# Kernel tuning notes

Measured on AMD Instinct MI355X. Metric: run time of the kernel, lower is better.

Reference implementation:

```python
import jax, jax.numpy as jnp
import numpy as np

N = 4096; IN = 78; OUT = 11
HN = 256; HB = 128; HM = 64; HV = 256; HU = 128
NOTES_PER_BEAT = 8; BEATS_PER_MEASURE = 4
NB = N // NOTES_PER_BEAT; NM = NB // BEATS_PER_MEASURE
UIN = 2*HN + 2*HB + 2*HM + 2*HV + OUT + 2 + 1 + 2   # output-LSTM input = 1424
BT_IN = 2*HB + 1 + 1 + 2 + 3 + (OUT - 1)            # tempo-LSTM input = 273
QPM_PRIMO_IDX = 5; TEMPO_IDX = 28


def _u(key, shape, k):
    return jax.random.uniform(key, shape, minval=-k, maxval=k, dtype=jnp.float32)


def _lstm_p(key, din, h, bidir):
    k = 1.0 / np.sqrt(h); n = 2 if bidir else 1
    k1, k2, k3 = jax.random.split(key, 3)
    Wi = _u(k1, (n, 4*h, din), k); Wh = _u(k2, (n, 4*h, h), k); b = _u(k3, (n, 4*h), k)
    if not bidir:
        Wi, Wh, b = Wi[0], Wh[0], b[0]
    return Wi, Wh, b


def _lin_p(key, din, dout):
    k = 1.0 / np.sqrt(din)
    k1, k2 = jax.random.split(key)
    return _u(k1, (dout, din), k), _u(k2, (dout,), k)


def setup_inputs():
    ks = jax.random.split(jax.random.key(0), 20)
    inp = {}
    inp['x'] = jax.random.normal(ks[0], (1, N, IN), dtype=jnp.float32)
    inp['y'] = jax.random.normal(ks[1], (1, 1, OUT), dtype=jnp.float32)
    inp['beat_ids'] = (jnp.arange(N) // NOTES_PER_BEAT).astype(jnp.int32)
    inp['measure_ids'] = (jnp.arange(N) // (NOTES_PER_BEAT * BEATS_PER_MEASURE)).astype(jnp.int32)
    inp['note_Wi'], inp['note_Wh'], inp['note_b'] = _lstm_p(ks[2], IN, HN, True)
    inp['voice_Wi'], inp['voice_Wh'], inp['voice_b'] = _lstm_p(ks[3], IN, HV, True)
    inp['beat_Wi'], inp['beat_Wh'], inp['beat_b'] = _lstm_p(ks[4], 2*HN, HB, True)
    inp['meas_Wi'], inp['meas_Wh'], inp['meas_b'] = _lstm_p(ks[5], 2*HB, HM, True)
    inp['Wba'], inp['bba'] = _lin_p(ks[6], 2*HN, 2*HN)
    inp['Wma'], inp['bma'] = _lin_p(ks[7], 2*HB, 2*HB)
    inp['Wta'], inp['bta'] = _lin_p(ks[8], OUT-1, OUT-1)
    inp['out_Wi'], inp['out_Wh'], inp['out_b'] = _lstm_p(ks[9], UIN, HU, False)
    inp['Wfc'], inp['bfc'] = _lin_p(ks[10], HU + UIN, OUT-1)
    inp['bt_Wi'], inp['bt_Wh'], inp['bt_b'] = _lstm_p(ks[11], BT_IN, HB, False)
    inp['Wt1'], inp['bt1'] = _lin_p(ks[12], HB, HB)
    inp['Wt2'], inp['bt2'] = _lin_p(ks[13], HB, 1)
    return inp


def _cell(h, c, xt, Wi, Wh, b):
    g = Wi @ xt + Wh @ h + b
    i, f, gg, o = jnp.split(g, 4)
    c2 = jax.nn.sigmoid(f) * c + jax.nn.sigmoid(i) * jnp.tanh(gg)
    return jax.nn.sigmoid(o) * jnp.tanh(c2), c2


def _lstm(xs, Wi, Wh, b, reverse=False):
    H = Wh.shape[-1]
    def step(carry, xt):
        h, c = _cell(carry[0], carry[1], xt, Wi, Wh, b)
        return (h, c), h
    init = (jnp.zeros(H, xs.dtype), jnp.zeros(H, xs.dtype))
    _, hs = jax.lax.scan(step, init, xs, reverse=reverse)
    return hs


def _bilstm(xs, Wi, Wh, b):
    return jnp.concatenate([_lstm(xs, Wi[0], Wh[0], b[0]),
                            _lstm(xs, Wi[1], Wh[1], b[1], reverse=True)], axis=-1)


def _seg_attn(h, seg, nseg, W, b):
    # sum_with_attention: softmax over group members, per feature dim (torch softmax dim=0)
    logits = h @ W.T + b
    m = jax.ops.segment_max(logits, seg, num_segments=nseg)
    e = jnp.exp(logits - m[seg])
    s = jax.ops.segment_sum(e, seg, num_segments=nseg)
    return jax.ops.segment_sum(h * (e / s[seg]), seg, num_segments=nseg)


def _forward(x, y, beat_ids, measure_ids, note_Wi, note_Wh, note_b, voice_Wi, voice_Wh, voice_b,
             beat_Wi, beat_Wh, beat_b, meas_Wi, meas_Wh, meas_b, Wba, bba, Wma, bma, Wta, bta,
             out_Wi, out_Wh, out_b, Wfc, bfc, bt_Wi, bt_Wh, bt_b, Wt1, bt1, Wt2, bt2):
    xs = x[0]                                   # [N, IN]
    note_h = _bilstm(xs, note_Wi, note_Wh, note_b)          # [N, 2*HN]
    voice_h = _bilstm(xs, voice_Wi, voice_Wh, voice_b)      # single voice -> whole seq
    beat_nodes = _seg_attn(note_h, beat_ids, NB, Wba, bba)  # [NB, 2*HN]
    beat_h = _bilstm(beat_nodes, beat_Wi, beat_Wh, beat_b)  # [NB, 2*HB]
    meas_of_beat = jax.ops.segment_min(measure_ids, beat_ids, num_segments=NB)
    meas_nodes = _seg_attn(beat_h, meas_of_beat, NM, Wma, bma)
    meas_h = _bilstm(meas_nodes, meas_Wi, meas_Wh, meas_b)  # [NM, 2*HM]

    qpm_primo = x[:, 0, QPM_PRIMO_IDX]          # (1,)
    tempo_primo = x[0, 0, -2:]                  # (2,)
    btv = xs[:, TEMPO_IDX:TEMPO_IDX+3]          # [N, 3]
    beat_pn = beat_h[beat_ids]                  # [N, 2*HB]
    meas_pn = meas_h[measure_ids]               # [N, 2*HM]
    is_b = jnp.concatenate([jnp.array([True]), beat_ids[1:] > beat_ids[:-1]])
    y_tail = y[0, 0, 1:]

    def step(carry, inp):
        buf, count, pt, th, tc, oh, oc, po, pv = carry
        nh_i, bh_i, mh_i, vh_i, btv_i, isb = inp
        # --- beat boundary: tempo attention + tempo LSTM step ---
        mask = jnp.arange(NOTES_PER_BEAT) < count
        logits = jnp.where(mask[:, None], buf @ Wta.T + bta, -1e9)
        att = jax.nn.softmax(logits, axis=0)
        result_node = jnp.where(count > 0, jnp.sum(buf * att, axis=0), y_tail)
        cat = jnp.concatenate([bh_i, pt, qpm_primo, tempo_primo, btv_i, result_node])
        nth, ntc = _cell(th, tc, cat, bt_Wi, bt_Wh, bt_b)
        tmp = Wt2 @ jax.nn.relu(Wt1 @ nth + bt1) + bt2     # (1,)
        th = jnp.where(isb, nth, th); tc = jnp.where(isb, ntc, tc)
        pt = jnp.where(isb, tmp, pt)
        buf = jnp.where(isb, jnp.zeros_like(buf), buf)
        count = jnp.where(isb, 0, count)
        comb = jnp.concatenate([nh_i, bh_i, mh_i, vh_i, po, pv, qpm_primo, tempo_primo])  # (UIN,)
        noh, noc = _cell(oh, oc, comb, out_Wi, out_Wh, out_b)
        out_fc = Wfc @ jnp.concatenate([noh, comb]) + bfc   # (OUT-1,)
        out = jnp.concatenate([pt, out_fc])                 # (OUT,)
        buf = buf.at[count].set(out_fc)
        return (buf, count + 1, pt, th, tc, noh, noc, out, out_fc[:2]), out

    carry0 = (jnp.zeros((NOTES_PER_BEAT, OUT-1)), jnp.array(0, jnp.int32), y[:, 0, 0],
              jnp.zeros(HB), jnp.zeros(HB), jnp.zeros(HU), jnp.zeros(HU), y[0, 0, :], jnp.zeros(2))
    _, outs = jax.lax.scan(step, carry0, (note_h, beat_pn, meas_pn, voice_h, btv, is_b))
    return outs[None], note_h[None]


def reference(x, y, beat_ids, measure_ids, note_Wi, note_Wh, note_b, voice_Wi, voice_Wh, voice_b,
              beat_Wi, beat_Wh, beat_b, meas_Wi, meas_Wh, meas_b, Wba, bba, Wma, bma, Wta, bta,
              out_Wi, out_Wh, out_b, Wfc, bfc, bt_Wi, bt_Wh, bt_b, Wt1, bt1, Wt2, bt2):
    return _forward(x, y, beat_ids, measure_ids, note_Wi, note_Wh, note_b, voice_Wi, voice_Wh, voice_b,
                    beat_Wi, beat_Wh, beat_b, meas_Wi, meas_Wh, meas_b, Wba, bba, Wma, bma, Wta, bta,
                    out_Wi, out_Wh, out_b, Wfc, bfc, bt_Wi, bt_Wh, bt_b, Wt1, bt1, Wt2, bt2)
```

## Files before the change

### kernel.cpp

```cpp
#include <hip/hip_runtime.h>
#include <hip/hip_bf16.h>

typedef unsigned int u32;
typedef _Float16 h16;
typedef __attribute__((ext_vector_type(2))) _Float16 h16x2;

union U4 { uint4 u; h16x2 p[4]; };
union U4H { uint4 u; h16 h[8]; };

static __device__ __forceinline__ float sigm(float x){ return 1.0f / (1.0f + __expf(-x)); }
static __device__ __forceinline__ float ftanh(float x){ return 1.0f - 2.0f/(1.0f + __expf(2.0f*x)); }
static __device__ __forceinline__ h16x2 f2h2(float a, float b){
  h16x2 r; r[0] = (h16)a; r[1] = (h16)b; return r;
}
static __device__ __forceinline__ void pinv(h16x2 &x){
  u32 t = __builtin_bit_cast(u32, x);
  asm volatile("" : "+v"(t));
  x = __builtin_bit_cast(h16x2, t);
}

#if defined(__has_builtin)
#if __has_builtin(__builtin_amdgcn_fdot2)
#define FDOT2_NATIVE 1
#endif
#endif
static __device__ __forceinline__ float fdot2(h16x2 a, h16x2 b, float c){
#ifdef FDOT2_NATIVE
  return __builtin_amdgcn_fdot2(a, b, c, false);
#else
  return c + (float)a[0]*(float)b[0] + (float)a[1]*(float)b[1];
#endif
}

#define NT 4096
#define OUTS_OFF 45056

__global__ __launch_bounds__(256) void k0_prep(
    const float* __restrict__ noteWh, const float* __restrict__ voiceWh,
    const float* __restrict__ outWi,  const float* __restrict__ Wfc,
    h16* __restrict__ WhF, h16* __restrict__ outWiF, h16* __restrict__ WfcKF)
{
  const int NWH = 4*1024*256;
  const int NOW = 512*1416;
  const int NFC = 10*1416;
  for (int i = blockIdx.x*256 + threadIdx.x; i < NWH + NOW + NFC; i += gridDim.x*256) {
    if (i < NWH) {
      int dir = i >> 18;
      int rem = i & 262143;
      const float* src = (dir < 2) ? noteWh : voiceWh;
      WhF[i] = (h16)src[((dir & 1) << 18) + rem];
    } else if (i < NWH + NOW) {
      int j = i - NWH;
      int r = j / 1416, c = j - r*1416;
      float v = 0.f;
      if (c < 1408) v = outWi[(size_t)r*1424 + c];
      else if (c < 1411) v = outWi[(size_t)r*1424 + 1421 + (c-1408)];
      outWiF[j] = (h16)v;
    } else {
      int j = i - NWH - NOW;
      int r = j / 1416, c = j - r*1416;
      float v = 0.f;
      if (c < 1408) v = Wfc[(size_t)r*1552 + 128 + c];
      else if (c < 1411) v = Wfc[(size_t)r*1552 + 1549 + (c-1408)];
      WfcKF[j] = (h16)v;
    }
  }
}

__global__ __launch_bounds__(256) void k1_xgates(
    const float* __restrict__ x,
    const float* __restrict__ noteWi, const float* __restrict__ noteB,
    const float* __restrict__ voiceWi, const float* __restrict__ voiceB,
    h16* __restrict__ preNV)
{
  const int dir = blockIdx.y;
  const int t0  = blockIdx.x * 16;
  const int tid = threadIdx.x;
  __shared__ float xs[16][80];
  for (int i = tid; i < 16*78; i += 256) {
    int tt = i / 78, j = i - tt*78;
    xs[tt][j] = x[(size_t)(t0+tt)*78 + j];
  }
  __syncthreads();
  const float* Wi = (dir < 2) ? noteWi : voiceWi;
  const float* B  = (dir < 2) ? noteB  : voiceB;
  const int dw = dir & 1;
  for (int gc = 0; gc < 4; ++gc) {
    int g = gc*256 + tid;
    const float* row = Wi + ((size_t)dw*1024 + g)*78;
    float bias = B[dw*1024 + g];
    float acc[16];
#pragma unroll
    for (int tt=0; tt<16; ++tt) acc[tt] = bias;
#pragma unroll 6
    for (int j=0; j<78; ++j) {
      float w = row[j];
#pragma unroll
      for (int tt=0; tt<16; ++tt)
        acc[tt] += w*xs[tt][j];
    }
#pragma unroll
    for (int tt=0; tt<16; ++tt)
      preNV[((size_t)dir*NT + (t0+tt))*1024 + (tid*4 + gc)] = (h16)acc[tt];
  }
}

__global__ __launch_bounds__(512, 2)
void k2_nvrec(
    const h16* __restrict__ WhF,
    const h16* __restrict__ preNV,
    float* __restrict__ note_h,
    float* __restrict__ voice_h,
    float* __restrict__ out_noteh)
{
  const int dir = blockIdx.x;
  const int L = threadIdx.x;
  const int lane = L & 63;
  const int wid  = L >> 6;
  const int hi   = lane >> 5;
  const int e    = wid*32 + (lane & 31);
  const int c0   = hi*128;
  const h16* Wb = WhF + (size_t)dir*1024*256;

  h16x2 w[4][48];
#pragma unroll
  for (int g=0; g<4; ++g) {
    const h16* row = Wb + (size_t)(g*256 + e)*256 + c0;
#pragma unroll
    for (int cb=0; cb<12; ++cb) {
      U4 a; a.u = *(const uint4*)(row + cb*8);
#pragma unroll
      for (int i=0;i<4;++i) w[g][cb*4+i] = a.p[i];
    }
  }
#pragma unroll
  for (int g=0; g<4; ++g)
#pragma unroll
    for (int c=0;c<48;++c) pinv(w[g][c]);

  __shared__ __align__(16) h16 Wl[4*4*2*256*8];
  __shared__ __align__(16) h16 hb[2][256];
#pragma unroll
  for (int cb=0; cb<4; ++cb)
#pragma unroll
    for (int g=0; g<4; ++g) {
      const h16* src = Wb + (size_t)(g*256 + e)*256 + c0 + 96 + cb*8;
      *(uint4*)&Wl[(size_t)((((cb*4+g)*2 + hi)*256 + e))*8] = *(const uint4*)src;
    }
  if (hi == 0) hb[0][e] = (h16)0.f;
  float cc = 0.f;
  __syncthreads();

  const bool fwd = ((dir & 1) == 0);
  const bool isNote = (dir < 2);
  float* hout = isNote ? note_h : voice_h;
  const int half = (dir & 1) * 256;
  const h16* pre = preNV + (size_t)dir*NT*1024;
  int cur = 0;
  const int step = fwd ? 1 : -1;
  int t = fwd ? 0 : NT-1;

  union PU { uint2 u; h16 h[4]; };
  PU pv_n; pv_n.u = *(const uint2*)(pre + (size_t)t*1024 + e*4);

  for (int it = 0; it < NT; ++it, t += step) {
    PU pv = pv_n;
    if (it+1 < NT) pv_n.u = *(const uint2*)(pre + (size_t)(t+step)*1024 + e*4);

    float ac[4][2] = {{0.f,0.f},{0.f,0.f},{0.f,0.f},{0.f,0.f}};
#pragma unroll
    for (int cb=0; cb<12; ++cb) {
      U4 hh; hh.u = *(const uint4*)&hb[cur][c0 + cb*8];
#pragma unroll
      for (int i=0;i<4;++i) {
        ac[0][i&1] = fdot2(w[0][cb*4+i], hh.p[i], ac[0][i&1]);
        ac[1][i&1] = fdot2(w[1][cb*4+i], hh.p[i], ac[1][i&1]);
        ac[2][i&1] = fdot2(w[2][cb*4+i], hh.p[i], ac[2][i&1]);
        ac[3][i&1] = fdot2(w[3][cb*4+i], hh.p[i], ac[3][i&1]);
      }
    }
#pragma unroll
    for (int cb=0; cb<4; ++cb) {
      U4 hh; hh.u = *(const uint4*)&hb[cur][c0 + 96 + cb*8];
#pragma unroll
      for (int g=0; g<4; ++g) {
        U4 wv; wv.u = *(const uint4*)&Wl[(size_t)((((cb*4+g)*2 + hi)*256 + e))*8];
#pragma unroll
        for (int i=0;i<4;++i) ac[g][i&1] = fdot2(wv.p[i], hh.p[i], ac[g][i&1]);
      }
    }
    float g4[4];
#pragma unroll
    for (int g=0; g<4; ++g) {
      float s = ac[g][0] + ac[g][1];
      s += __shfl_xor(s, 32, 64);
      g4[g] = s;
    }
    float gi = (float)pv.h[0] + g4[0];
    float gf = (float)pv.h[1] + g4[1];
    float gg = (float)pv.h[2] + g4[2];
    float go = (float)pv.h[3] + g4[3];
    cc = sigm(gf)*cc + sigm(gi)*ftanh(gg);
    float h = sigm(go)*ftanh(cc);
    if (hi == 0) {
      hb[cur^1][e] = (h16)h;
      hout[(size_t)t*512 + half + e] = h;
      if (isNote) out_noteh[(size_t)t*512 + half + e] = h;
    }
    cur ^= 1;
    __syncthreads();
  }
}

__global__ __launch_bounds__(256) void k3_battn(
    const float* __restrict__ note_h,
    const float* __restrict__ Wba, const float* __restrict__ bba,
    float* __restrict__ beat_nodes)
{
  const int b = blockIdx.x;
  const int tid = threadIdx.x;
  __shared__ float nh[8][512];
  for (int i = tid; i < 8*512; i += 256)
    nh[i>>9][i&511] = note_h[(size_t)b*8*512 + i];
  __syncthreads();
  for (int dc = 0; dc < 2; ++dc) {
    int d = dc*256 + tid;
    const float* wr = Wba + (size_t)d*512;
    float bb = bba[d];
    float l[8];
#pragma unroll
    for (int n=0;n<8;++n) l[n]=bb;
#pragma unroll 4
    for (int j=0; j<512; ++j) {
      float w = wr[j];
#pragma unroll
      for (int n=0;n<8;++n) l[n] += w*nh[n][j];
    }
    float m = l[0];
#pragma unroll
    for (int n=1;n<8;++n) m = fmaxf(m, l[n]);
    float s = 0.f, o = 0.f;
#pragma unroll
    for (int n=0;n<8;++n) { float e = __expf(l[n]-m); s += e; o += e*nh[n][d]; }
    beat_nodes[(size_t)b*512 + d] = o / s;
  }
}

__global__ __launch_bounds__(256) void k4_bgates(
    const float* __restrict__ beat_nodes,
    const float* __restrict__ beatWi, const float* __restrict__ beatB,
    float* __restrict__ preB)
{
  const int dir = blockIdx.y, b0 = blockIdx.x*8, tid = threadIdx.x;
  __shared__ float nd[8][512];
  for (int i = tid; i < 8*512; i += 256)
    nd[i>>9][i&511] = beat_nodes[(size_t)b0*512 + i];
  __syncthreads();
  for (int gc = 0; gc < 2; ++gc) {
    int g = gc*256 + tid;
    const float* wr = beatWi + ((size_t)dir*512 + g)*512;
    float bias = beatB[dir*512 + g];
    float acc[8];
#pragma unroll
    for (int n=0;n<8;++n) acc[n]=bias;
#pragma unroll 4
    for (int j=0; j<512; ++j) {
      float w = wr[j];
#pragma unroll
      for (int n=0;n<8;++n) acc[n] += w*nd[n][j];
    }
#pragma unroll
    for (int n=0;n<8;++n)
      preB[((size_t)dir*512 + (b0+n))*512 + g] = acc[n];
  }
}

__global__ __launch_bounds__(512) void k5_brec(
    const float* __restrict__ beatWh,
    const float* __restrict__ preB,
    float* __restrict__ beat_h)
{
  const int dir = blockIdx.x, L = threadIdx.x;
  h16x2 w[64];
  {
    const float2* p = (const float2*)(beatWh + ((size_t)dir*512 + L)*128);
#pragma unroll
    for (int c=0;c<64;++c){
      float2 v = p[c];
      w[c] = f2h2(v.x, v.y);
    }
  }
#pragma unroll
  for (int c=0;c<64;++c) pinv(w[c]);
  __shared__ __align__(16) h16 hb[128];
  __shared__ float gl[512];
  if (L < 128) hb[L] = (h16)0.f;
  float cc = 0.f;
  __syncthreads();
  const bool fwd = (dir == 0);
  for (int it = 0; it < 512; ++it) {
    const int t = fwd ? it : 511 - it;
    float pr = preB[((size_t)dir*512 + t)*512 + L];
    float ac[4] = {0.f,0.f,0.f,0.f};
#pragma unroll
    for (int c=0;c<16;++c){
      U4 hh; hh.u = *(const uint4*)&hb[c*8];
#pragma unroll
      for (int i=0;i<4;++i) ac[i] = fdot2(w[c*4+i], hh.p[i], ac[i]);
    }
    gl[L] = pr + ((ac[0]+ac[1]) + (ac[2]+ac[3]));
    __syncthreads();
    if (L < 128) {
      float gi = gl[L], gf = gl[L+128], gg = gl[L+256], go = gl[L+384];
      cc = sigm(gf)*cc + sigm(gi)*ftanh(gg);
      float h = sigm(go)*ftanh(cc);
      hb[L] = (h16)h;
      beat_h[(size_t)t*256 + dir*128 + L] = h;
    }
    __syncthreads();
  }
}

__global__ __launch_bounds__(256) void k6_mattn(
    const float* __restrict__ beat_h,
    const float* __restrict__ Wma, const float* __restrict__ bma,
    float* __restrict__ meas_nodes)
{
  const int m = blockIdx.x, tid = threadIdx.x;
  __shared__ float bh[4][256];
  for (int i = tid; i < 4*256; i += 256)
    bh[i>>8][i&255] = beat_h[(size_t)m*4*256 + i];
  __syncthreads();
  int d = tid;
  const float* wr = Wma + (size_t)d*256;
  float bb = bma[d];
  float l[4];
#pragma unroll
  for (int n=0;n<4;++n) l[n]=bb;
#pragma unroll 4
  for (int j=0; j<256; ++j) {
    float w = wr[j];
#pragma unroll
    for (int n=0;n<4;++n) l[n] += w*bh[n][j];
  }
  float mm = fmaxf(fmaxf(l[0],l[1]), fmaxf(l[2],l[3]));
  float s = 0.f, o = 0.f;
#pragma unroll
  for (int n=0;n<4;++n) { float e = __expf(l[n]-mm); s += e; o += e*bh[n][d]; }
  meas_nodes[(size_t)m*256 + d] = o / s;
}

__global__ __launch_bounds__(256) void k7_mgates(
    const float* __restrict__ meas_nodes,
    const float* __restrict__ measWi, const float* __restrict__ measB,
    float* __restrict__ preM)
{
  const int dir = blockIdx.y, m0 = blockIdx.x*8, tid = threadIdx.x;
  __shared__ float nd[8][256];
  for (int i = tid; i < 8*256; i += 256)
    nd[i>>8][i&255] = meas_nodes[(size_t)m0*256 + i];
  __syncthreads();
  int g = tid;
  const float* wr = measWi + ((size_t)dir*256 + g)*256;
  float bias = measB[dir*256 + g];
  float acc[8];
#pragma unroll
  for (int n=0;n<8;++n) acc[n]=bias;
#pragma unroll 4
  for (int j=0; j<256; ++j) {
    float w = wr[j];
#pragma unroll
    for (int n=0;n<8;++n) acc[n] += w*nd[n][j];
  }
#pragma unroll
  for (int n=0;n<8;++n)
    preM[((size_t)dir*128 + (m0+n))*256 + g] = acc[n];
}

__global__ __launch_bounds__(256, 2) void k8_mrec(
    const float* __restrict__ measWh,
    const float* __restrict__ preM,
    float* __restrict__ meas_h)
{
  const int dir = blockIdx.x, L = threadIdx.x;
  h16x2 w[32];
  {
    const float2* p = (const float2*)(measWh + ((size_t)dir*256 + L)*64);
#pragma unroll
    for (int c=0;c<32;++c){
      float2 v = p[c];
      w[c] = f2h2(v.x, v.y);
    }
  }
#pragma unroll
  for (int c=0;c<32;++c) pinv(w[c]);
  __shared__ __align__(16) h16 hb[64];
  __shared__ float gl[256];
  if (L < 64) hb[L] = (h16)0.f;
  float cc = 0.f;
  __syncthreads();
  const bool fwd = (dir == 0);
  for (int it = 0; it < 128; ++it) {
    const int t = fwd ? it : 127 - it;
    float pr = preM[((size_t)dir*128 + t)*256 + L];
    float ac[4] = {0.f,0.f,0.f,0.f};
#pragma unroll
    for (int c=0;c<8;++c){
      U4 hh; hh.u = *(const uint4*)&hb[c*8];
#pragma unroll
      for (int i=0;i<4;++i) ac[i] = fdot2(w[c*4+i], hh.p[i], ac[i]);
    }
    gl[L] = pr + ((ac[0]+ac[1]) + (ac[2]+ac[3]));
    __syncthreads();
    if (L < 64) {
      float gi = gl[L], gf = gl[L+64], gg = gl[L+128], go = gl[L+192];
      cc = sigm(gf)*cc + sigm(gi)*ftanh(gg);
      float h = sigm(go)*ftanh(cc);
      hb[L] = (h16)h;
      meas_h[(size_t)t*128 + dir*64 + L] = h;
    }
    __syncthreads();
  }
}

__global__ __launch_bounds__(256) void k9_scanpre(
    const float* __restrict__ note_h, const float* __restrict__ voice_h,
    const float* __restrict__ beat_h, const float* __restrict__ meas_h,
    const float* __restrict__ xf,
    const h16* __restrict__ outWiF, const h16* __restrict__ WfcKF,
    const float* __restrict__ outB, const float* __restrict__ bfc,
    float* __restrict__ pre_out, float* __restrict__ pre_fc)
{
  const int t0 = blockIdx.x*8, tid = threadIdx.x;
  __shared__ __align__(16) h16 kn[8][1416];
  const float qpm = xf[5], tp0 = xf[76], tp1 = xf[77];
  for (int i = tid; i < 8*1416; i += 256) {
    int tt = i/1416, c = i - tt*1416;
    int t = t0 + tt;
    float v;
    if (c < 512) v = note_h[(size_t)t*512 + c];
    else if (c < 768) v = beat_h[(size_t)(t>>3)*256 + (c-512)];
    else if (c < 896) v = meas_h[(size_t)(t>>5)*128 + (c-768)];
    else if (c < 1408) v = voice_h[(size_t)t*512 + (c-896)];
    else if (c == 1408) v = qpm;
    else if (c == 1409) v = tp0;
    else if (c == 1410) v = tp1;
    else v = 0.f;
    kn[tt][c] = (h16)v;
  }
  __syncthreads();
  for (int rr = 0; rr < 3; ++rr) {
    int r = (rr < 2) ? (tid + rr*256) : (512 + tid);
    if (rr == 2 && tid >= 10) break;
    const h16* wrow = (r < 512) ? (outWiF + (size_t)r*1416) : (WfcKF + (size_t)(r-512)*1416);
    float bias = (r < 512) ? outB[r] : bfc[r-512];
    float acc[8];
#pragma unroll
    for (int tt=0;tt<8;++tt) acc[tt] = bias;
    for (int cu = 0; cu < 177; ++cu) {
      U4 wv; wv.u = *(const uint4*)(wrow + cu*8);
#pragma unroll
      for (int tt=0; tt<8; ++tt) {
        U4 kv; kv.u = *(const uint4*)&kn[tt][cu*8];
#pragma unroll
        for (int i=0;i<4;++i) acc[tt] = fdot2(wv.p[i], kv.p[i], acc[tt]);
      }
    }
#pragma unroll
    for (int tt=0; tt<8; ++tt) {
      if (r < 512) pre_out[((size_t)(t0+tt)*128 + (r & 127))*4 + (r >> 7)] = acc[tt];
      else pre_fc[(size_t)(t0+tt)*16 + (r-512)] = acc[tt];
    }
  }
}

__global__ __launch_bounds__(256) void k9b_btpre(
    const float* __restrict__ beat_h, const float* __restrict__ xf,
    const float* __restrict__ btWi, const float* __restrict__ btB,
    float* __restrict__ pre_bt)
{
  const int b0 = blockIdx.x*8, tid = threadIdx.x;
  __shared__ float bh[8][256];
  __shared__ float btv[8][3];
  for (int i = tid; i < 8*256; i += 256)
    bh[i>>8][i&255] = beat_h[(size_t)b0*256 + i];
  if (tid < 24) {
    int n = tid/3, j = tid - n*3;
    btv[n][j] = xf[(size_t)(b0+n)*8*78 + 28 + j];
  }
  __syncthreads();
  const float qpm = xf[5], tp0 = xf[76], tp1 = xf[77];
  for (int gc = 0; gc < 2; ++gc) {
    int g = gc*256 + tid;
    const float* row = btWi + (size_t)g*273;
    float bias = btB[g];
    float acc[8];
#pragma unroll
    for (int n=0;n<8;++n) acc[n]=bias;
#pragma unroll 4
    for (int j = 0; j < 256; ++j) {
      float w = row[j];
#pragma unroll
      for (int n=0;n<8;++n) acc[n] += w*bh[n][j];
    }
    float w257 = row[257], w258 = row[258], w259 = row[259];
    float w260 = row[260], w261 = row[261], w262 = row[262];
#pragma unroll
    for (int n=0;n<8;++n) {
      acc[n] += w257*qpm + w258*tp0 + w259*tp1
              + w260*btv[n][0] + w261*btv[n][1] + w262*btv[n][2];
      pre_bt[((size_t)(b0+n)*128 + (g & 127))*4 + (g >> 7)] = acc[n];
    }
  }
}

__global__ __launch_bounds__(512) __attribute__((amdgpu_waves_per_eu(2, 2)))
void k10_scan(
    const float* __restrict__ pre_out, const float* __restrict__ pre_fc,
    const float* __restrict__ pre_bt,
    const float* __restrict__ outWh, const float* __restrict__ btWh,
    const float* __restrict__ outWi, const float* __restrict__ btWi,
    const float* __restrict__ Wfc,
    const float* __restrict__ Wta, const float* __restrict__ bta,
    const float* __restrict__ Wt1, const float* __restrict__ bt1,
    const float* __restrict__ Wt2, const float* __restrict__ bt2,
    const float* __restrict__ yf,
    float* __restrict__ out)
{
  const int L = threadIdx.x;
  const int lane = L & 63;
  const int wid  = L >> 6;
  const int jl   = lane & 15;
  const int q    = lane >> 4;
  const int j    = wid*16 + jl;
  const int row  = q*128 + j;

  h16x2 owh[4][16], btw[4][16];
#pragma unroll
  for (int g=0; g<4; ++g) {
    const float2* p  = (const float2*)(outWh + (size_t)(g*128 + j)*128 + q*32);
    const float2* pb = (const float2*)(btWh  + (size_t)(g*128 + j)*128 + q*32);
#pragma unroll
    for (int c=0;c<16;++c){
      float2 a = p[c];  owh[g][c] = f2h2(a.x, a.y);
      float2 b = pb[c]; btw[g][c] = f2h2(b.x, b.y);
    }
  }
#pragma unroll
  for (int g=0; g<4; ++g)
#pragma unroll
    for (int c=0;c<16;++c) pinv(owh[g][c]);

  float oseq[13];
#pragma unroll
  for (int jj=0;jj<13;++jj) oseq[jj] = outWi[(size_t)row*1424 + 1408 + jj];
  float btpt = btWi[(size_t)row*273 + 256];
  float btrn[10];
#pragma unroll
  for (int d=0;d<10;++d) btrn[d] = btWi[(size_t)row*273 + 263 + d];

  __shared__ __align__(16) h16 oh16[128];
  __shared__ __align__(16) h16 th16[128];
  __shared__ __align__(16) h16 Wt1f[128*136];
  __shared__ __align__(16) h16 WfcD[10*128];
  __shared__ __align__(16) float pofc[16];
  __shared__ float ptvS;
  __shared__ float buf[8][10];
  __shared__ float rn[10], att[8][10], r1v[128], ytail[10];
  __shared__ float WfcSeq[10][13];
  __shared__ float WtaS[100], btaS[10], Wt2S[128], bt1S[128], bt2S;

  for (int i=L; i<128*128; i+=512) Wt1f[(i>>7)*136 + (i&127)] = (h16)Wt1[i];
  for (int i=L; i<10*128; i+=512)  WfcD[i] = (h16)Wfc[(size_t)(i>>7)*1552 + (i&127)];
  if (L < 100) WtaS[L] = Wta[L];
  if (L < 10)  btaS[L] = bta[L];
  if (L < 128) { Wt2S[L] = Wt2[L]; bt1S[L] = bt1[L]; }
  if (L == 0)  bt2S = bt2[0];
  if (L < 128) { oh16[L] = (h16)0.f; th16[L] = (h16)0.f; }
  if (L < 11) pofc[L] = yf[L];
  if (L >= 11 && L < 16) pofc[L] = 0.f;
  if (L == 0) ptvS = yf[0];
  if (L < 10) ytail[L] = yf[1+L];
  if (L < 80) buf[L/10][L%10] = 0.f;
  if (L < 130) WfcSeq[L/13][L%13] = Wfc[(size_t)(L/13)*1552 + 1536 + (L%13)];
  float oc = 0.f, tc = 0.f;
  float ac4[4]  = {0.f,0.f,0.f,0.f};
  float acB4[4] = {0.f,0.f,0.f,0.f};
  const int dD = L >> 2, qD = L & 3;
  const float* ppo = pre_out + (size_t)j*4 + q;
  const float* ppb = pre_bt  + (size_t)j*4 + q;
  float prv  = *ppo; ppo += 512;
  float prbt = *ppb; ppb += 512;
  float prfc = (L < 40 && qD == 0) ? pre_fc[dD] : 0.f;
  const float* pp_fc = pre_fc + 16 + dD;
  __syncthreads();

  for (int t = 0; t < NT; ++t) {
    const bool isb = (t & 7) == 0;
    if (isb) {
      if (t == 0) {
        if (L < 10) rn[L] = ytail[L];
      } else {
        if (L < 80) {
          int n = L/10, d = L - n*10;
          float s = btaS[d];
#pragma unroll
          for (int jj=0;jj<10;++jj) s += buf[n][jj]*WtaS[d*10 + jj];
          att[n][d] = s;
        }
        __syncthreads();
        if (L < 10) {
          float m = att[0][L];
#pragma unroll
          for (int n=1;n<8;++n) m = fmaxf(m, att[n][L]);
          float s = 0.f, acc = 0.f;
#pragma unroll
          for (int n=0;n<8;++n) { float e = __expf(att[n][L]-m); s += e; acc += e*buf[n][L]; }
          rn[L] = acc/s;
        }
      }
      __syncthreads();
    }
    {
      float4 pf0 = *(const float4*)&pofc[0];
      float4 pf1 = *(const float4*)&pofc[4];
      float4 pf2 = *(const float4*)&pofc[8];
      float  pcc = pofc[12];
      float ex = prv;
      ex += oseq[0]*pf0.x + oseq[1]*pf0.y + oseq[2]*pf0.z + oseq[3]*pf0.w;
      ex += oseq[4]*pf1.x + oseq[5]*pf1.y + oseq[6]*pf1.z + oseq[7]*pf1.w;
      ex += oseq[8]*pf2.x + oseq[9]*pf2.y + oseq[10]*pf2.z + oseq[11]*pf2.w;
      ex += oseq[12]*pcc;
      prv = *ppo; ppo += 512;
      float p0 = ac4[0] + ((q==0) ? ex : 0.f);
      float p1 = ac4[1] + ((q==1) ? ex : 0.f);
      float p2 = ac4[2] + ((q==2) ? ex : 0.f);
      float p3 = ac4[3] + ((q==3) ? ex : 0.f);
      p0 += __shfl_xor(p0, 16, 64); p0 += __shfl_xor(p0, 32, 64);
      p1 += __shfl_xor(p1, 16, 64); p1 += __shfl_xor(p1, 32, 64);
      p2 += __shfl_xor(p2, 16, 64); p2 += __shfl_xor(p2, 32, 64);
      p3 += __shfl_xor(p3, 16, 64); p3 += __shfl_xor(p3, 32, 64);
      oc = sigm(p1)*oc + sigm(p0)*ftanh(p2);
      float nh = sigm(p3)*ftanh(oc);
      if (q == 0) oh16[j] = (h16)nh;
    }
    if (isb) {
      float ex = prbt + btpt*ptvS;
#pragma unroll
      for (int d=0;d<10;++d) ex += btrn[d]*rn[d];
      prbt = *ppb; ppb += 512;
      float p0 = acB4[0] + ((q==0) ? ex : 0.f);
      float p1 = acB4[1] + ((q==1) ? ex : 0.f);
      float p2 = acB4[2] + ((q==2) ? ex : 0.f);
      float p3 = acB4[3] + ((q==3) ? ex : 0.f);
      p0 += __shfl_xor(p0, 16, 64); p0 += __shfl_xor(p0, 32, 64);
      p1 += __shfl_xor(p1, 16, 64); p1 += __shfl_xor(p1, 32, 64);
      p2 += __shfl_xor(p2, 16, 64); p2 += __shfl_xor(p2, 32, 64);
      p3 += __shfl_xor(p3, 16, 64); p3 += __shfl_xor(p3, 32, 64);
      tc = sigm(p1)*tc + sigm(p0)*ftanh(p2);
      float nth = sigm(p3)*ftanh(tc);
      if (q == 0) th16[j] = (h16)nth;
    }
    __syncthreads();
    {
      float a0=0.f,a1=0.f,a2=0.f,a3=0.f;
#pragma unroll
      for (int cb=0; cb<4; ++cb) {
        U4 hh; hh.u = *(const uint4*)&oh16[q*32 + cb*8];
#pragma unroll
        for (int i=0;i<4;++i) {
          a0 = fdot2(owh[0][cb*4+i], hh.p[i], a0);
          a1 = fdot2(owh[1][cb*4+i], hh.p[i], a1);
          a2 = fdot2(owh[2][cb*4+i], hh.p[i], a2);
          a3 = fdot2(owh[3][cb*4+i], hh.p[i], a3);
        }
      }
      ac4[0]=a0; ac4[1]=a1; ac4[2]=a2; ac4[3]=a3;
    }
    if (((t+1) & 7) == 0) {
      float b0=0.f,b1=0.f,b2=0.f,b3=0.f;
#pragma unroll
      for (int cb=0; cb<4; ++cb) {
        U4 hh; hh.u = *(const uint4*)&th16[q*32 + cb*8];
#pragma unroll
        for (int i=0;i<4;++i) {
          b0 = fdot2(btw[0][cb*4+i], hh.p[i], b0);
          b1 = fdot2(btw[1][cb*4+i], hh.p[i], b1);
          b2 = fdot2(btw[2][cb*4+i], hh.p[i], b2);
          b3 = fdot2(btw[3][cb*4+i], hh.p[i], b3);
        }
      }
      acB4[0]=b0; acB4[1]=b1; acB4[2]=b2; acB4[3]=b3;
    }
    if (isb) {
      if (L < 128) {
        float ac[4] = {0.f,0.f,0.f,0.f};
        const h16* wrow = &Wt1f[L*136];
#pragma unroll
        for (int k=0;k<16;++k){
          U4 wv; wv.u = *(const uint4*)(wrow + k*8);
          U4 hh; hh.u = *(const uint4*)&th16[k*8];
#pragma unroll
          for (int i=0;i<4;++i) ac[i] = fdot2(wv.p[i], hh.p[i], ac[i]);
        }
        float s = bt1S[L] + ((ac[0]+ac[1]) + (ac[2]+ac[3]));
        r1v[L] = fmaxf(s, 0.f);
      }
      __syncthreads();
    }
    if (L < 64) {
      float ptv_l;
      if (isb) {
        float p = Wt2S[L]*r1v[L] + Wt2S[L+64]*r1v[L+64];
#pragma unroll
        for (int sft=32; sft>0; sft>>=1) p += __shfl_xor(p, sft, 64);
        ptv_l = p + bt2S;
        if (L == 0) ptvS = ptv_l;
      } else {
        ptv_l = ptvS;
      }
      float s = 0.f;
      if (L < 40) {
        const h16* wr = &WfcD[dD*128 + qD*32];
#pragma unroll
        for (int k=0;k<4;++k){
          U4H wv; wv.u = *(const uint4*)(wr + k*8);
          U4H hh; hh.u = *(const uint4*)&oh16[qD*32 + k*8];
#pragma unroll
          for (int i=0;i<8;++i) s += (float)wv.h[i] * (float)hh.h[i];
        }
      }
      s += __shfl_xor(s, 1, 64);
      s += __shfl_xor(s, 2, 64);
      float e = 0.f;
      if (L < 40 && qD == 0) {
        e = prfc;
#pragma unroll
        for (int jj=0;jj<13;++jj) e += WfcSeq[dD][jj]*pofc[jj];
        prfc = *pp_fc; pp_fc += 16;
      }
      float ofc = s + e;
      int srcE = (L >= 1 && L < 11) ? 4*(L-1) : ((L >= 11 && L < 13) ? 4*(L-11) : 0);
      float valE = __shfl(ofc, srcE, 64);
      float bval = __shfl(ofc, 4*(L & 15), 64);
      if (L == 0)      { out[(size_t)t*11] = ptv_l; pofc[0] = ptv_l; }
      else if (L < 11) { out[(size_t)t*11 + L] = valE; pofc[L] = valE; }
      else if (L < 13) { pofc[L] = valE; }
      if (L < 10) buf[t & 7][L] = bval;
    }
    __syncthreads();
  }
}

extern "C" void kernel_launch(void* const* d_in, const int* in_sizes, int n_in,
                              void* d_out, int out_size, void* d_ws, size_t ws_size,
                              hipStream_t stream)
{
  const float* x      = (const float*)d_in[0];
  const float* y      = (const float*)d_in[1];
  const float* noteWi = (const float*)d_in[4];
  const float* noteWh = (const float*)d_in[5];
  const float* noteB  = (const float*)d_in[6];
  const float* voiceWi= (const float*)d_in[7];
  const float* voiceWh= (const float*)d_in[8];
  const float* voiceB = (const float*)d_in[9];
  const float* beatWi = (const float*)d_in[10];
  const float* beatWh = (const float*)d_in[11];
  const float* beatB  = (const float*)d_in[12];
  const float* measWi = (const float*)d_in[13];
  const float* measWh = (const float*)d_in[14];
  const float* measB  = (const float*)d_in[15];
  const float* Wba    = (const float*)d_in[16];
  const float* bba    = (const float*)d_in[17];
  const float* Wma    = (const float*)d_in[18];
  const float* bma    = (const float*)d_in[19];
  const float* Wta    = (const float*)d_in[20];
  const float* bta    = (const float*)d_in[21];
  const float* outWi  = (const float*)d_in[22];
  const float* outWh  = (const float*)d_in[23];
  const float* outB   = (const float*)d_in[24];
  const float* Wfc    = (const float*)d_in[25];
  const float* bfc    = (const float*)d_in[26];
  const float* btWi   = (const float*)d_in[27];
  const float* btWh   = (const float*)d_in[28];
  const float* btB    = (const float*)d_in[29];
  const float* Wt1    = (const float*)d_in[30];
  const float* bt1    = (const float*)d_in[31];
  const float* Wt2    = (const float*)d_in[32];
  const float* bt2    = (const float*)d_in[33];

  float* fws = (float*)d_ws;
  float* note_h     = fws + 0;
  float* voice_h    = fws + 2097152;
  float* beat_nodes = fws + 4194304;
  float* preB       = fws + 4456448;
  float* beat_h     = fws + 4980736;
  float* meas_nodes = fws + 5111808;
  float* preM       = fws + 5144576;
  float* meas_h     = fws + 5210112;
  float* pre_out    = fws + 5226496;
  float* pre_fc     = fws + 7323648;
  float* pre_bt     = fws + 7389184;
  h16* hws   = (h16*)(fws + 7651328);
  h16* preNV  = hws;
  h16* WhF    = hws + 16777216;
  h16* outWiF = hws + 17825792;
  h16* WfcKF  = hws + 18550784;

  float* out_outs  = (float*)d_out;
  float* out_noteh = out_outs + OUTS_OFF;

  hipLaunchKernelGGL(k0_prep, dim3(1024), dim3(256), 0, stream,
                     noteWh, voiceWh, outWi, Wfc, WhF, outWiF, WfcKF);
  hipLaunchKernelGGL(k1_xgates, dim3(256,4), dim3(256), 0, stream,
                     x, noteWi, noteB, voiceWi, voiceB, preNV);
  hipLaunchKernelGGL(k2_nvrec, dim3(4), dim3(512), 0, stream,
                     WhF, preNV, note_h, voice_h, out_noteh);
  hipLaunchKernelGGL(k3_battn, dim3(512), dim3(256), 0, stream,
                     note_h, Wba, bba, beat_nodes);
  hipLaunchKernelGGL(k4_bgates, dim3(64,2), dim3(256), 0, stream,
                     beat_nodes, beatWi, beatB, preB);
  hipLaunchKernelGGL(k5_brec, dim3(2), dim3(512), 0, stream,
                     beatWh, preB, beat_h);
  hipLaunchKernelGGL(k6_mattn, dim3(128), dim3(256), 0, stream,
                     beat_h, Wma, bma, meas_nodes);
  hipLaunchKernelGGL(k7_mgates, dim3(16,2), dim3(256), 0, stream,
                     meas_nodes, measWi, measB, preM);
  hipLaunchKernelGGL(k8_mrec, dim3(2), dim3(256), 0, stream,
                     measWh, preM, meas_h);
  hipLaunchKernelGGL(k9b_btpre, dim3(64), dim3(256), 0, stream,
                     beat_h, x, btWi, btB, pre_bt);
  hipLaunchKernelGGL(k9_scanpre, dim3(512), dim3(256), 0, stream,
                     note_h, voice_h, beat_h, meas_h, x, outWiF, WfcKF, outB, bfc, pre_out, pre_fc);
  hipLaunchKernelGGL(k10_scan, dim3(1), dim3(512), 0, stream,
                     pre_out, pre_fc, pre_bt, outWh, btWh, outWi, btWi, Wfc,
                     Wta, bta, Wt1, bt1, Wt2, bt2, y, out_outs);
}
```

Measured before the change: 13.99 ms.

## Replicate output-FC epilogue per wave and double-buffer hidden state to drop barrier

Every wave now computes the FC output and previous-output feedback redundantly, keeping them in registers and broadcasting with lane shuffles instead of going through shared memory. The note-level hidden state is double-buffered so the end-of-step __syncthreads can be removed. A barrier is added only on beat steps, and the Wt1 relu layer is moved earlier. This cuts one block-wide barrier per timestep on the serial recurrence, at the cost of duplicated FC arithmetic in every wave and extra register pressure.

```diff
diff --git a/kernel.cpp b/kernel.cpp
--- a/kernel.cpp
+++ b/kernel.cpp
@@ -559,12 +559,11 @@
 #pragma unroll
   for (int d=0;d<10;++d) btrn[d] = btWi[(size_t)row*273 + 263 + d];
 
-  __shared__ __align__(16) h16 oh16[128];
+  __shared__ __align__(16) h16 oh16[2][128];
   __shared__ __align__(16) h16 th16[128];
   __shared__ __align__(16) h16 Wt1f[128*136];
   __shared__ __align__(16) h16 WfcD[10*128];
-  __shared__ __align__(16) float pofc[16];
-  __shared__ float ptvS;
+  __shared__ float ptvInit;
   __shared__ float buf[8][10];
   __shared__ float rn[10], att[8][10], r1v[128], ytail[10];
   __shared__ float WfcSeq[10][13];
@@ -576,23 +575,27 @@
   if (L < 10)  btaS[L] = bta[L];
   if (L < 128) { Wt2S[L] = Wt2[L]; bt1S[L] = bt1[L]; }
   if (L == 0)  bt2S = bt2[0];
-  if (L < 128) { oh16[L] = (h16)0.f; th16[L] = (h16)0.f; }
-  if (L < 11) pofc[L] = yf[L];
-  if (L >= 11 && L < 16) pofc[L] = 0.f;
-  if (L == 0) ptvS = yf[0];
+  if (L < 128) { oh16[0][L] = (h16)0.f; th16[L] = (h16)0.f; }
+  if (L == 0)  ptvInit = yf[0];
   if (L < 10) ytail[L] = yf[1+L];
   if (L < 80) buf[L/10][L%10] = 0.f;
   if (L < 130) WfcSeq[L/13][L%13] = Wfc[(size_t)(L/13)*1552 + 1536 + (L%13)];
   float oc = 0.f, tc = 0.f;
   float ac4[4]  = {0.f,0.f,0.f,0.f};
   float acB4[4] = {0.f,0.f,0.f,0.f};
-  const int dD = L >> 2, qD = L & 3;
+  const int dD = lane >> 2, qD = lane & 3;
   const float* ppo = pre_out + (size_t)j*4 + q;
   const float* ppb = pre_bt  + (size_t)j*4 + q;
   float prv  = *ppo; ppo += 512;
   float prbt = *ppb; ppb += 512;
-  float prfc = (L < 40 && qD == 0) ? pre_fc[dD] : 0.f;
+  float prfc = (lane < 40 && qD == 0) ? pre_fc[dD] : 0.f;
   const float* pp_fc = pre_fc + 16 + dD;
+  float pR[13];
+#pragma unroll
+  for (int jj=0;jj<11;++jj) pR[jj] = yf[jj];
+  pR[11] = 0.f; pR[12] = 0.f;
+  float ptvR = yf[0];
+  int cur = 0;
   __syncthreads();
 
   for (int t = 0; t < NT; ++t) {
@@ -601,6 +604,7 @@
       if (t == 0) {
         if (L < 10) rn[L] = ytail[L];
       } else {
+        __syncthreads();
         if (L < 80) {
           int n = L/10, d = L - n*10;
           float s = btaS[d];
@@ -622,15 +626,11 @@
       __syncthreads();
     }
     {
-      float4 pf0 = *(const float4*)&pofc[0];
-      float4 pf1 = *(const float4*)&pofc[4];
-      float4 pf2 = *(const float4*)&pofc[8];
-      float  pcc = pofc[12];
       float ex = prv;
-      ex += oseq[0]*pf0.x + oseq[1]*pf0.y + oseq[2]*pf0.z + oseq[3]*pf0.w;
-      ex += oseq[4]*pf1.x + oseq[5]*pf1.y + oseq[6]*pf1.z + oseq[7]*pf1.w;
-      ex += oseq[8]*pf2.x + oseq[9]*pf2.y + oseq[10]*pf2.z + oseq[11]*pf2.w;
-      ex += oseq[12]*pcc;
+      ex += oseq[0]*pR[0] + oseq[1]*pR[1] + oseq[2]*pR[2] + oseq[3]*pR[3];
+      ex += oseq[4]*pR[4] + oseq[5]*pR[5] + oseq[6]*pR[6] + oseq[7]*pR[7];
+      ex += oseq[8]*pR[8] + oseq[9]*pR[9] + oseq[10]*pR[10] + oseq[11]*pR[11];
+      ex += oseq[12]*pR[12];
       prv = *ppo; ppo += 512;
       float p0 = ac4[0] + ((q==0) ? ex : 0.f);
       float p1 = ac4[1] + ((q==1) ? ex : 0.f);
@@ -642,10 +642,10 @@
       p3 += __shfl_xor(p3, 16, 64); p3 += __shfl_xor(p3, 32, 64);
       oc = sigm(p1)*oc + sigm(p0)*ftanh(p2);
       float nh = sigm(p3)*ftanh(oc);
-      if (q == 0) oh16[j] = (h16)nh;
+      if (q == 0) oh16[cur^1][j] = (h16)nh;
     }
     if (isb) {
-      float ex = prbt + btpt*ptvS;
+      float ex = prbt + btpt*ptvR;
 #pragma unroll
       for (int d=0;d<10;++d) ex += btrn[d]*rn[d];
       prbt = *ppb; ppb += 512;
@@ -662,11 +662,27 @@
       if (q == 0) th16[j] = (h16)nth;
     }
     __syncthreads();
+    if (isb) {
+      if (L < 128) {
+        float ac[4] = {0.f,0.f,0.f,0.f};
+        const h16* wrow = &Wt1f[L*136];
+#pragma unroll
+        for (int k=0;k<16;++k){
+          U4 wv; wv.u = *(const uint4*)(wrow + k*8);
+          U4 hh; hh.u = *(const uint4*)&th16[k*8];
+#pragma unroll
+          for (int i=0;i<4;++i) ac[i] = fdot2(wv.p[i], hh.p[i], ac[i]);
+        }
+        float s = bt1S[L] + ((ac[0]+ac[1]) + (ac[2]+ac[3]));
+        r1v[L] = fmaxf(s, 0.f);
+      }
+      __syncthreads();
+    }
     {
       float a0=0.f,a1=0.f,a2=0.f,a3=0.f;
 #pragma unroll
       for (int cb=0; cb<4; ++cb) {
-        U4 hh; hh.u = *(const uint4*)&oh16[q*32 + cb*8];
+        U4 hh; hh.u = *(const uint4*)&oh16[cur^1][q*32 + cb*8];
 #pragma unroll
         for (int i=0;i<4;++i) {
           a0 = fdot2(owh[0][cb*4+i], hh.p[i], a0);
@@ -693,39 +709,19 @@
       acB4[0]=b0; acB4[1]=b1; acB4[2]=b2; acB4[3]=b3;
     }
     if (isb) {
-      if (L < 128) {
-        float ac[4] = {0.f,0.f,0.f,0.f};
-        const h16* wrow = &Wt1f[L*136];
-#pragma unroll
-        for (int k=0;k<16;++k){
-          U4 wv; wv.u = *(const uint4*)(wrow + k*8);
-          U4 hh; hh.u = *(const uint4*)&th16[k*8];
-#pragma unroll
-          for (int i=0;i<4;++i) ac[i] = fdot2(wv.p[i], hh.p[i], ac[i]);
-        }
-        float s = bt1S[L] + ((ac[0]+ac[1]) + (ac[2]+ac[3]));
-        r1v[L] = fmaxf(s, 0.f);
-      }
-      __syncthreads();
-    }
-    if (L < 64) {
-      float ptv_l;
-      if (isb) {
-        float p = Wt2S[L]*r1v[L] + Wt2S[L+64]*r1v[L+64];
-#pragma unroll
-        for (int sft=32; sft>0; sft>>=1) p += __shfl_xor(p, sft, 64);
-        ptv_l = p + bt2S;
-        if (L == 0) ptvS = ptv_l;
-      } else {
-        ptv_l = ptvS;
-      }
+      float p = Wt2S[lane]*r1v[lane] + Wt2S[lane+64]*r1v[lane+64];
+#pragma unroll
+      for (int sft=32; sft>0; sft>>=1) p += __shfl_xor(p, sft, 64);
+      ptvR = p + bt2S;
+    }
+    {
       float s = 0.f;
-      if (L < 40) {
+      if (lane < 40) {
         const h16* wr = &WfcD[dD*128 + qD*32];
 #pragma unroll
         for (int k=0;k<4;++k){
           U4H wv; wv.u = *(const uint4*)(wr + k*8);
-          U4H hh; hh.u = *(const uint4*)&oh16[qD*32 + k*8];
+          U4H hh; hh.u = *(const uint4*)&oh16[cur^1][qD*32 + k*8];
 #pragma unroll
           for (int i=0;i<8;++i) s += (float)wv.h[i] * (float)hh.h[i];
         }
@@ -733,22 +729,32 @@
       s += __shfl_xor(s, 1, 64);
       s += __shfl_xor(s, 2, 64);
       float e = 0.f;
-      if (L < 40 && qD == 0) {
+      if (lane < 40 && qD == 0) {
         e = prfc;
 #pragma unroll
-        for (int jj=0;jj<13;++jj) e += WfcSeq[dD][jj]*pofc[jj];
+        for (int jj=0;jj<13;++jj) e += WfcSeq[dD][jj]*pR[jj];
         prfc = *pp_fc; pp_fc += 16;
       }
       float ofc = s + e;
-      int srcE = (L >= 1 && L < 11) ? 4*(L-1) : ((L >= 11 && L < 13) ? 4*(L-11) : 0);
-      float valE = __shfl(ofc, srcE, 64);
-      float bval = __shfl(ofc, 4*(L & 15), 64);
-      if (L == 0)      { out[(size_t)t*11] = ptv_l; pofc[0] = ptv_l; }
-      else if (L < 11) { out[(size_t)t*11 + L] = valE; pofc[L] = valE; }
-      else if (L < 13) { pofc[L] = valE; }
-      if (L < 10) buf[t & 7][L] = bval;
-    }
-    __syncthreads();
+      float f0 = __shfl(ofc,  0, 64), f1 = __shfl(ofc,  4, 64);
+      float f2 = __shfl(ofc,  8, 64), f3 = __shfl(ofc, 12, 64);
+      float f4 = __shfl(ofc, 16, 64), f5 = __shfl(ofc, 20, 64);
+      float f6 = __shfl(ofc, 24, 64), f7 = __shfl(ofc, 28, 64);
+      float f8 = __shfl(ofc, 32, 64), f9 = __shfl(ofc, 36, 64);
+      if (wid == 0) {
+        int srcE = (lane >= 1 && lane < 11) ? 4*(lane-1) : 0;
+        float valE = __shfl(ofc, srcE, 64);
+        float bval = __shfl(ofc, 4*(lane & 15), 64);
+        if (lane == 0)      out[(size_t)t*11] = ptvR;
+        else if (lane < 11) out[(size_t)t*11 + lane] = valE;
+        if (lane < 10) buf[t & 7][lane] = bval;
+      }
+      pR[0] = ptvR;
+      pR[1] = f0; pR[2] = f1; pR[3] = f2; pR[4] = f3; pR[5] = f4;
+      pR[6] = f5; pR[7] = f6; pR[8] = f7; pR[9] = f8; pR[10] = f9;
+      pR[11] = f0; pR[12] = f1;
+    }
+    cur ^= 1;
   }
 }
 
```

New measurement: 15.13 ms. 8.1% more time.
